# Kernel optimization log

Hardware: AMD Instinct MI355X
Metric: run time of the kernel (lower is better)

## Reference

```python
import jax, jax.numpy as jnp
import numpy as np

DIM = 128
NH = 4
K = 7
PAD = K // 2  # dilation = 1
MLP_HID = 4 * DIM
EPS = 1e-5


def _layernorm(x, w, b):
    m = jnp.mean(x, axis=-1, keepdims=True)
    v = jnp.mean((x - m) ** 2, axis=-1, keepdims=True)
    return (x - m) / jnp.sqrt(v + EPS) * w + b


def _windows(xp, H, W):
    # xp: [B, nh, Hp, Wp, hd] zero-padded; returns [B, nh, H, W, hd, K*K]
    return jnp.stack(
        [xp[:, :, i:i + H, j:j + W, :] for i in range(K) for j in range(K)],
        axis=-1,
    )


def setup_inputs() -> dict:
    key = jax.random.key(0)
    ks = jax.random.split(key, 10)
    s = 0.02
    inp = {
        "x": jax.random.normal(ks[0], (4, 56, 56, DIM), dtype=jnp.float32),
        "ln1_w": jnp.ones((DIM,), jnp.float32),
        "ln1_b": jnp.zeros((DIM,), jnp.float32),
        "w_qkv": jax.random.normal(ks[1], (DIM, 3 * DIM), jnp.float32) * s,
        "b_qkv": jnp.zeros((3 * DIM,), jnp.float32),
        "rpb": jax.random.normal(ks[2], (NH, K * K), jnp.float32) * s,
        "w_proj": jax.random.normal(ks[3], (DIM, DIM), jnp.float32) * s,
        "b_proj": jnp.zeros((DIM,), jnp.float32),
        "ln2_w": jnp.ones((DIM,), jnp.float32),
        "ln2_b": jnp.zeros((DIM,), jnp.float32),
        "w_fc1": jax.random.normal(ks[4], (DIM, MLP_HID), jnp.float32) * s,
        "b_fc1": jnp.zeros((MLP_HID,), jnp.float32),
        "w_fc2": jax.random.normal(ks[5], (MLP_HID, DIM), jnp.float32) * s,
        "b_fc2": jnp.zeros((DIM,), jnp.float32),
    }
    return inp


def _nat_block(x, ln1_w, ln1_b, w_qkv, b_qkv, rpb, w_proj, b_proj,
               ln2_w, ln2_b, w_fc1, b_fc1, w_fc2, b_fc2):
    B, H, W, C = x.shape
    hd = C // NH
    scale = hd ** -0.5

    # --- neighborhood attention ---
    xn = _layernorm(x, ln1_w, ln1_b)
    qkv = xn @ w_qkv + b_qkv                       # [B,H,W,3C]
    qkv = qkv.reshape(B, H, W, 3, NH, hd)
    qkv = jnp.transpose(qkv, (3, 0, 4, 1, 2, 5))   # [3,B,nh,H,W,hd]
    q, k, v = qkv[0] * scale, qkv[1], qkv[2]
    # zero-pad spatial dims (matches F.pad with constant 0 in original)
    pad = ((0, 0), (0, 0), (PAD, PAD), (PAD, PAD), (0, 0))
    kp = jnp.pad(k, pad)
    vp = jnp.pad(v, pad)
    kw = _windows(kp, H, W)                        # [B,nh,H,W,hd,49]
    vw = _windows(vp, H, W)
    attn = jnp.einsum('bnhwd,bnhwdk->bnhwk', q, kw)
    attn = attn + rpb[None, :, None, None, :]
    attn = jax.nn.softmax(attn, axis=-1)
    out = jnp.einsum('bnhwk,bnhwdk->bnhwd', attn, vw)  # [B,nh,H,W,hd]
    out = jnp.transpose(out, (0, 2, 3, 1, 4)).reshape(B, H, W, C)
    x = x + (out @ w_proj + b_proj)

    # --- MLP ---
    xn2 = _layernorm(x, ln2_w, ln2_b)
    h = jax.nn.gelu(xn2 @ w_fc1 + b_fc1, approximate=False)
    x = x + (h @ w_fc2 + b_fc2)
    return x


def reference(x, ln1_w, ln1_b, w_qkv, b_qkv, rpb, w_proj, b_proj,
              ln2_w, ln2_b, w_fc1, b_fc1, w_fc2, b_fc2):
    return _nat_block(x, ln1_w, ln1_b, w_qkv, b_qkv, rpb, w_proj, b_proj,
                      ln2_w, ln2_b, w_fc1, b_fc1, w_fc2, b_fc2)
```

## Files before the change

kernel.cpp:

```cpp
#include <hip/hip_runtime.h>

using bf16x8 = __attribute__((ext_vector_type(8))) short;
using f32x4  = __attribute__((ext_vector_type(4))) float;
typedef unsigned short u16;
typedef __attribute__((ext_vector_type(8))) unsigned short u16x8;

__device__ __forceinline__ u16 f2b(float f){
  unsigned int i=__float_as_uint(f);
  return (u16)((i + 0x7FFFu + ((i>>16)&1u))>>16);
}
__device__ __forceinline__ float b2f(u16 u){
  union{unsigned int i; float f;}v; v.i=((unsigned int)u)<<16; return v.f;
}
__device__ __forceinline__ void async16(const void* g, void* l){
  __builtin_amdgcn_global_load_lds((__attribute__((address_space(1))) void*)(g),
                                   (__attribute__((address_space(3))) void*)(l), 16, 0, 0);
}
__device__ __forceinline__ float gelu_tanh(float v){
  float u = v*(0.7978845608f + 0.0356774081f*v*v);
  float e = __expf(-2.0f*fabsf(u));
  float th = (1.0f-e)/(1.0f+e);
  th = (u<0.f)? -th : th;
  return 0.5f*v*(1.0f+th);
}

__global__ void prep_kernel(const float* __restrict__ wqkv, const float* __restrict__ wproj,
                            const float* __restrict__ wfc1, const float* __restrict__ wfc2,
                            u16* __restrict__ tqkv, u16* __restrict__ tproj,
                            u16* __restrict__ tfc1, u16* __restrict__ tfc2)
{
  int idx = blockIdx.x*256 + threadIdx.x;
  if (idx < 49152){ int n=idx>>7, k=idx&127; tqkv[idx]=f2b(wqkv[k*384+n]); }
  else if (idx < 65536){ int t=idx-49152; int n=t>>7, k=t&127; tproj[t]=f2b(wproj[k*128+n]); }
  else if (idx < 131072){ int t=idx-65536; int n=t>>7, k=t&127; tfc1[t]=f2b(wfc1[k*512+n]); }
  else if (idx < 196608){ int t=idx-131072; int n=t>>9, k=t&511; tfc2[t]=f2b(wfc2[k*128+n]); }
}

__global__ __launch_bounds__(256)
void qkv_ln_kernel(const float* __restrict__ x,
                   const float* __restrict__ ln1w, const float* __restrict__ ln1b,
                   const u16* __restrict__ tqkv, const float* __restrict__ bqkv,
                   u16* __restrict__ qb, u16* __restrict__ kb, u16* __restrict__ vb)
{
  __shared__ __align__(16) char smem[49152];
  char* lA = smem;
  char* lB = smem + 16384;

  const int tid = threadIdx.x;
  const int lane = tid&63, wid = tid>>6;
  const int quad = lane>>4, lrow = lane&15;
  const int m0 = blockIdx.x*64;
  const int wm = (wid&1)*32, wn = (wid>>1)*64;

  {
    const int row = tid>>2, q = tid&3;
    float xv[32];
    const float4* xr = (const float4*)(x + (size_t)(m0+row)*128 + q*32);
    float s=0.f, sq=0.f;
    #pragma unroll
    for (int c4=0;c4<8;c4++){
      float4 t = xr[c4];
      xv[c4*4]=t.x; xv[c4*4+1]=t.y; xv[c4*4+2]=t.z; xv[c4*4+3]=t.w;
      s += t.x+t.y+t.z+t.w;
      sq += t.x*t.x+t.y*t.y+t.z*t.z+t.w*t.w;
    }
    s  += __shfl_xor(s,1);  s  += __shfl_xor(s,2);
    sq += __shfl_xor(sq,1); sq += __shfl_xor(sq,2);
    float mean = s*0.0078125f;
    float rstd = rsqrtf(sq*0.0078125f - mean*mean + 1e-5f);
    const float4* wr = (const float4*)(ln1w + q*32);
    const float4* br = (const float4*)(ln1b + q*32);
    u16 nv[32];
    #pragma unroll
    for (int c4=0;c4<8;c4++){
      float4 w4 = wr[c4], b4 = br[c4];
      nv[c4*4]   = f2b((xv[c4*4]  -mean)*rstd*w4.x + b4.x);
      nv[c4*4+1] = f2b((xv[c4*4+1]-mean)*rstd*w4.y + b4.y);
      nv[c4*4+2] = f2b((xv[c4*4+2]-mean)*rstd*w4.z + b4.z);
      nv[c4*4+3] = f2b((xv[c4*4+3]-mean)*rstd*w4.w + b4.w);
    }
    #pragma unroll
    for (int cc=0;cc<4;cc++){
      u16x8 pk;
      #pragma unroll
      for (int e=0;e<8;e++) pk[e] = nv[cc*8+e];
      *(u16x8*)(lA + (((q*4+cc)*64 + row)<<4)) = pk;
    }
  }

  for (int nc=0; nc<3; nc++){
    __syncthreads();
    #pragma unroll
    for (int kk=0;kk<8;kk++){
      int i = tid + kk*256;
      int n = i&127, c = i>>7;
      async16(tqkv + (size_t)(nc*128+n)*128 + c*8, lB + i*16);
    }
    __syncthreads();

    f32x4 acc[2][4] = {};
    #pragma unroll
    for (int ks=0;ks<4;ks++){
      bf16x8 af[2], bfr[4];
      #pragma unroll
      for (int i=0;i<2;i++) af[i]  = ((const bf16x8*)lA)[(ks*4+quad)*64  + wm + i*16 + lrow];
      #pragma unroll
      for (int j=0;j<4;j++) bfr[j] = ((const bf16x8*)lB)[(ks*4+quad)*128 + wn + j*16 + lrow];
      #pragma unroll
      for (int i=0;i<2;i++)
        #pragma unroll
        for (int j=0;j<4;j++)
          acc[i][j] = __builtin_amdgcn_mfma_f32_16x16x32_bf16(af[i], bfr[j], acc[i][j], 0,0,0);
    }

    const float scale = 0.17677669529663687f;
    u16* dst = (nc==0)? qb : ((nc==1)? kb : vb);
    #pragma unroll
    for (int j=0;j<4;j++){
      int col = wn + j*16 + lrow;
      float bia = bqkv[nc*128 + col];
      #pragma unroll
      for (int i=0;i<2;i++){
        #pragma unroll
        for (int r=0;r<4;r++){
          int row = m0 + wm + i*16 + quad*4 + r;
          float val = acc[i][j][r] + bia;
          if (nc==0) val *= scale;
          dst[(size_t)row*128 + col] = f2b(val);
        }
      }
    }
  }
}

__global__ __launch_bounds__(256)
void attn_kernel(const u16* __restrict__ qb, const u16* __restrict__ kb,
                 const u16* __restrict__ vb, const float* __restrict__ rpb,
                 u16* __restrict__ aout)
{
  __shared__ __align__(16) u16 kt[196*32];
  __shared__ __align__(16) u16 vt[196*32];

  const int tid = threadIdx.x;
  const int tile = blockIdx.x;
  const int bh = blockIdx.y;
  const int b = bh>>2, h = bh&3;
  const int ty = (tile/7)*8, tx = (tile%7)*8;

  #pragma unroll
  for (int k=0;k<4;k++){
    int i = tid + k*256;
    if (i < 784){
      int pos = i>>2, c = i&3;
      int ly = pos/14, lx = pos-ly*14;
      int gy = ty + ly - 3, gx = tx + lx - 3;
      float4 kv = {0,0,0,0}, vv = {0,0,0,0};
      if (gy>=0 && gy<56 && gx>=0 && gx<56){
        size_t base = ((size_t)(b*3136 + gy*56 + gx)*128 + h*32 + c*8);
        kv = *(const float4*)(kb + base);
        vv = *(const float4*)(vb + base);
      }
      ((float4*)kt)[i] = kv;
      ((float4*)vt)[i] = vv;
    }
  }
  __syncthreads();

  const int px = tid>>2, q = tid&3;
  const int ly = px>>3, lx = px&7;
  const int tok = b*3136 + (ty+ly)*56 + (tx+lx);
  const int nbase = (ly*14 + lx)*32 + q*8;

  float qv[8];
  { u16x8 qq = *(const u16x8*)(qb + (size_t)tok*128 + h*32 + q*8);
    #pragma unroll
    for (int i=0;i<8;i++) qv[i]=b2f(qq[i]); }

  float sc[49];
  #pragma unroll
  for (int ky=0;ky<7;ky++){
    #pragma unroll
    for (int kx=0;kx<7;kx++){
      int n = ky*7+kx;
      u16x8 kk = *(const u16x8*)(kt + nbase + (ky*14+kx)*32);
      float s = 0.f;
      #pragma unroll
      for (int i=0;i<8;i++) s += qv[i]*b2f(kk[i]);
      s += __shfl_xor(s,1); s += __shfl_xor(s,2);
      sc[n] = s + rpb[h*49+n];
    }
  }
  float m=-1e30f;
  #pragma unroll
  for (int n=0;n<49;n++) m = fmaxf(m, sc[n]);
  float l=0.f;
  #pragma unroll
  for (int n=0;n<49;n++){ sc[n]=__expf(sc[n]-m); l+=sc[n]; }
  float inv = 1.f/l;

  float o[8]={};
  #pragma unroll
  for (int ky=0;ky<7;ky++){
    #pragma unroll
    for (int kx=0;kx<7;kx++){
      int n = ky*7+kx;
      u16x8 vv = *(const u16x8*)(vt + nbase + (ky*14+kx)*32);
      float p = sc[n];
      #pragma unroll
      for (int i=0;i<8;i++) o[i] += p*b2f(vv[i]);
    }
  }
  u16x8 ov;
  #pragma unroll
  for (int i=0;i<8;i++) ov[i] = f2b(o[i]*inv);
  *(u16x8*)(aout + (size_t)tok*128 + h*32 + q*8) = ov;
}

__global__ __launch_bounds__(256)
void mega_mlp_kernel(const u16* __restrict__ aout, const float* __restrict__ x,
                     const u16* __restrict__ tproj, const float* __restrict__ bproj,
                     const float* __restrict__ ln2w, const float* __restrict__ ln2b,
                     const u16* __restrict__ tfc1, const float* __restrict__ bfc1,
                     const u16* __restrict__ tfc2, const float* __restrict__ bfc2,
                     float* __restrict__ out)
{
  __shared__ __align__(16) char smem[65536];
  char* lA  = smem;
  char* lB  = smem + 16384;
  char* xn2 = smem + 49152;

  const int tid = threadIdx.x;
  const int lane = tid&63, wid = tid>>6;
  const int quad = lane>>4, lrow = lane&15;
  const int m0 = blockIdx.x*64;
  const int wm = (wid&1)*32, wn = (wid>>1)*64;
  const int half = wid>>1;

  #pragma unroll
  for (int kk=0;kk<4;kk++){
    int i = tid + kk*256;
    int row = i&63, c = i>>6;
    async16(aout + (size_t)(m0+row)*128 + c*8, lA + i*16);
  }
  #pragma unroll
  for (int kk=0;kk<8;kk++){
    int i = tid + kk*256;
    int n = i&127, c = i>>7;
    async16(tproj + (size_t)n*128 + c*8, lB + i*16);
  }
  __syncthreads();

  f32x4 acc[2][4] = {};
  #pragma unroll
  for (int ks=0;ks<4;ks++){
    bf16x8 af[2], bfr[4];
    #pragma unroll
    for (int i=0;i<2;i++) af[i]  = ((const bf16x8*)lA)[(ks*4+quad)*64  + wm + i*16 + lrow];
    #pragma unroll
    for (int j=0;j<4;j++) bfr[j] = ((const bf16x8*)lB)[(ks*4+quad)*128 + wn + j*16 + lrow];
    #pragma unroll
    for (int i=0;i<2;i++)
      #pragma unroll
      for (int j=0;j<4;j++)
        acc[i][j] = __builtin_amdgcn_mfma_f32_16x16x32_bf16(af[i], bfr[j], acc[i][j], 0,0,0);
  }
  __syncthreads();

  float x1v[2][4][4];
  float ps[2][4] = {}, pq[2][4] = {};
  #pragma unroll
  for (int j=0;j<4;j++){
    int col = wn + j*16 + lrow;
    float bia = bproj[col];
    #pragma unroll
    for (int i=0;i<2;i++){
      #pragma unroll
      for (int r=0;r<4;r++){
        int row = m0 + wm + i*16 + quad*4 + r;
        float val = acc[i][j][r] + bia + x[(size_t)row*128 + col];
        x1v[i][j][r] = val;
        ps[i][r] += val; pq[i][r] += val*val;
      }
    }
  }
  #pragma unroll
  for (int i=0;i<2;i++)
    #pragma unroll
    for (int r=0;r<4;r++){
      #pragma unroll
      for (int off=1; off<16; off<<=1){
        ps[i][r] += __shfl_xor(ps[i][r], off);
        pq[i][r] += __shfl_xor(pq[i][r], off);
      }
    }
  float* redS = (float*)lA;
  float* redQ = redS + 128;
  if (lrow==0){
    #pragma unroll
    for (int i=0;i<2;i++)
      #pragma unroll
      for (int r=0;r<4;r++){
        int row = wm + i*16 + quad*4 + r;
        redS[half*64 + row] = ps[i][r];
        redQ[half*64 + row] = pq[i][r];
      }
  }
  __syncthreads();

  {
    float w2[4], b2[4];
    #pragma unroll
    for (int j=0;j<4;j++){ int col = wn+j*16+lrow; w2[j]=ln2w[col]; b2[j]=ln2b[col]; }
    #pragma unroll
    for (int i=0;i<2;i++){
      #pragma unroll
      for (int r=0;r<4;r++){
        int row = wm + i*16 + quad*4 + r;
        float mean = (redS[row] + redS[64+row])*0.0078125f;
        float var  = (redQ[row] + redQ[64+row])*0.0078125f - mean*mean;
        float rstd = rsqrtf(var + 1e-5f);
        #pragma unroll
        for (int j=0;j<4;j++){
          int col = wn + j*16 + lrow;
          u16 hv = f2b((x1v[i][j][r]-mean)*rstd*w2[j] + b2[j]);
          ((u16*)xn2)[((col>>3)*64 + row)*8 + (col&7)] = hv;
        }
      }
    }
  }
  __syncthreads();

  f32x4 acc3[2][4] = {};
  for (int nc=0; nc<4; nc++){
    if (nc>0) __syncthreads();
    #pragma unroll
    for (int kk=0;kk<8;kk++){
      int i = tid + kk*256;
      int n = i&127, c = i>>7;
      async16(tfc1 + (size_t)(nc*128+n)*128 + c*8, lB + i*16);
    }
    __syncthreads();

    f32x4 acc2[2][4] = {};
    #pragma unroll
    for (int ks=0;ks<4;ks++){
      bf16x8 af[2], bfr[4];
      #pragma unroll
      for (int i=0;i<2;i++) af[i]  = ((const bf16x8*)xn2)[(ks*4+quad)*64  + wm + i*16 + lrow];
      #pragma unroll
      for (int j=0;j<4;j++) bfr[j] = ((const bf16x8*)lB)[(ks*4+quad)*128 + wn + j*16 + lrow];
      #pragma unroll
      for (int i=0;i<2;i++)
        #pragma unroll
        for (int j=0;j<4;j++)
          acc2[i][j] = __builtin_amdgcn_mfma_f32_16x16x32_bf16(af[i], bfr[j], acc2[i][j], 0,0,0);
    }
    #pragma unroll
    for (int j=0;j<4;j++){
      int col = wn + j*16 + lrow;
      float bia = bfc1[nc*128 + col];
      #pragma unroll
      for (int i=0;i<2;i++){
        #pragma unroll
        for (int r=0;r<4;r++){
          int row = wm + i*16 + quad*4 + r;
          float g = gelu_tanh(acc2[i][j][r] + bia);
          ((u16*)lA)[((col>>3)*64 + row)*8 + (col&7)] = f2b(g);
        }
      }
    }
    __syncthreads();
    #pragma unroll
    for (int kk=0;kk<8;kk++){
      int i = tid + kk*256;
      int n = i&127, c = i>>7;
      async16(tfc2 + (size_t)n*512 + nc*128 + c*8, lB + i*16);
    }
    __syncthreads();

    #pragma unroll
    for (int ks=0;ks<4;ks++){
      bf16x8 af[2], bfr[4];
      #pragma unroll
      for (int i=0;i<2;i++) af[i]  = ((const bf16x8*)lA)[(ks*4+quad)*64  + wm + i*16 + lrow];
      #pragma unroll
      for (int j=0;j<4;j++) bfr[j] = ((const bf16x8*)lB)[(ks*4+quad)*128 + wn + j*16 + lrow];
      #pragma unroll
      for (int i=0;i<2;i++)
        #pragma unroll
        for (int j=0;j<4;j++)
          acc3[i][j] = __builtin_amdgcn_mfma_f32_16x16x32_bf16(af[i], bfr[j], acc3[i][j], 0,0,0);
    }
  }

  #pragma unroll
  for (int j=0;j<4;j++){
    int col = wn + j*16 + lrow;
    float bia = bfc2[col];
    #pragma unroll
    for (int i=0;i<2;i++){
      #pragma unroll
      for (int r=0;r<4;r++){
        int row = m0 + wm + i*16 + quad*4 + r;
        out[(size_t)row*128 + col] = acc3[i][j][r] + bia + x1v[i][j][r];
      }
    }
  }
}

extern "C" void kernel_launch(void* const* d_in, const int* in_sizes, int n_in,
                              void* d_out, int out_size, void* d_ws, size_t ws_size,
                              hipStream_t stream)
{
  const float* x     =(const float*)d_in[0];
  const float* ln1w  =(const float*)d_in[1];
  const float* ln1b  =(const float*)d_in[2];
  const float* wqkv  =(const float*)d_in[3];
  const float* bqkv  =(const float*)d_in[4];
  const float* rpb   =(const float*)d_in[5];
  const float* wproj =(const float*)d_in[6];
  const float* bproj =(const float*)d_in[7];
  const float* ln2w  =(const float*)d_in[8];
  const float* ln2b  =(const float*)d_in[9];
  const float* wfc1  =(const float*)d_in[10];
  const float* bfc1  =(const float*)d_in[11];
  const float* wfc2  =(const float*)d_in[12];
  const float* bfc2  =(const float*)d_in[13];

  char* ws=(char*)d_ws;
  size_t o=0;
  u16* tqkv =(u16*)(ws+o); o+=98304;
  u16* tproj=(u16*)(ws+o); o+=32768;
  u16* tfc1 =(u16*)(ws+o); o+=131072;
  u16* tfc2 =(u16*)(ws+o); o+=131072;
  u16* aout =(u16*)(ws+o); o+=3211264;
  u16* qb   =(u16*)(ws+o); o+=3211264;
  u16* kb   =(u16*)(ws+o); o+=3211264;
  u16* vb   =(u16*)(ws+o); o+=3211264;

  prep_kernel<<<768,256,0,stream>>>(wqkv,wproj,wfc1,wfc2,tqkv,tproj,tfc1,tfc2);
  qkv_ln_kernel<<<196,256,0,stream>>>(x,ln1w,ln1b,tqkv,bqkv,qb,kb,vb);
  attn_kernel<<<dim3(49,16),256,0,stream>>>(qb,kb,vb,rpb,aout);
  mega_mlp_kernel<<<196,256,0,stream>>>(aout,x,tproj,bproj,ln2w,ln2b,
                                        tfc1,bfc1,tfc2,bfc2,(float*)d_out);
}
```

Measured before the change: 158.0 us.

## Compute neighborhood attention with MFMA over a banded 2-row halo window

Rewrites the neighborhood attention kernel so each wavefront handles 16 query pixels (two tile rows) and computes QK^T and PV with bf16 MFMA against the 112 halo positions those rows can reach. Out-of-window positions are masked to -inf before softmax, and probabilities are staged in LDS as bf16. V is stored transposed with padded strides so it can feed the MFMA B operand. This replaces scalar FMA dot products and shuffle reductions with matrix instructions. In exchange it does redundant masked work, about 112 candidate positions per query instead of 49, and adds the cost of LDS transposes and rounding P to bf16.

Measured after the change: 142.3 us. 1.11x faster.

```diff
diff --git a/kernel.cpp b/kernel.cpp
--- a/kernel.cpp
+++ b/kernel.cpp
@@ -4,6 +4,7 @@
 using f32x4  = __attribute__((ext_vector_type(4))) float;
 typedef unsigned short u16;
 typedef __attribute__((ext_vector_type(8))) unsigned short u16x8;
+typedef __attribute__((ext_vector_type(4))) unsigned short u16x4;
 
 __device__ __forceinline__ u16 f2b(float f){
   unsigned int i=__float_as_uint(f);
@@ -133,87 +134,137 @@
   }
 }
 
+#define KT_S 40
+#define VT_S 232
+#define P_S  152
 __global__ __launch_bounds__(256)
 void attn_kernel(const u16* __restrict__ qb, const u16* __restrict__ kb,
                  const u16* __restrict__ vb, const float* __restrict__ rpb,
                  u16* __restrict__ aout)
 {
-  __shared__ __align__(16) u16 kt[196*32];
-  __shared__ __align__(16) u16 vt[196*32];
+  __shared__ __align__(16) char smem[50192];
+  u16*  kt   = (u16*)smem;
+  u16*  vt   = (u16*)(smem + 15680);
+  u16*  Pm   = (u16*)(smem + 30528);
+  float* srpb= (float*)(smem + 49984);
 
   const int tid = threadIdx.x;
-  const int tile = blockIdx.x;
-  const int bh = blockIdx.y;
+  const int tile = blockIdx.x, bh = blockIdx.y;
   const int b = bh>>2, h = bh&3;
   const int ty = (tile/7)*8, tx = (tile%7)*8;
-
-  #pragma unroll
-  for (int k=0;k<4;k++){
-    int i = tid + k*256;
+  const int lane = tid&63, wid = tid>>6;
+  const int quad = lane>>4, lrow = lane&15;
+
+  #pragma unroll
+  for (int kk=0;kk<4;kk++){
+    int i = tid + kk*256;
     if (i < 784){
-      int pos = i>>2, c = i&3;
-      int ly = pos/14, lx = pos-ly*14;
-      int gy = ty + ly - 3, gx = tx + lx - 3;
-      float4 kv = {0,0,0,0}, vv = {0,0,0,0};
-      if (gy>=0 && gy<56 && gx>=0 && gx<56){
-        size_t base = ((size_t)(b*3136 + gy*56 + gx)*128 + h*32 + c*8);
-        kv = *(const float4*)(kb + base);
-        vv = *(const float4*)(vb + base);
-      }
-      ((float4*)kt)[i] = kv;
-      ((float4*)vt)[i] = vv;
-    }
-  }
-  __syncthreads();
-
-  const int px = tid>>2, q = tid&3;
-  const int ly = px>>3, lx = px&7;
-  const int tok = b*3136 + (ty+ly)*56 + (tx+lx);
-  const int nbase = (ly*14 + lx)*32 + q*8;
-
-  float qv[8];
-  { u16x8 qq = *(const u16x8*)(qb + (size_t)tok*128 + h*32 + q*8);
-    #pragma unroll
-    for (int i=0;i<8;i++) qv[i]=b2f(qq[i]); }
-
-  float sc[49];
-  #pragma unroll
-  for (int ky=0;ky<7;ky++){
-    #pragma unroll
-    for (int kx=0;kx<7;kx++){
-      int n = ky*7+kx;
-      u16x8 kk = *(const u16x8*)(kt + nbase + (ky*14+kx)*32);
-      float s = 0.f;
-      #pragma unroll
-      for (int i=0;i<8;i++) s += qv[i]*b2f(kk[i]);
-      s += __shfl_xor(s,1); s += __shfl_xor(s,2);
-      sc[n] = s + rpb[h*49+n];
-    }
-  }
-  float m=-1e30f;
-  #pragma unroll
-  for (int n=0;n<49;n++) m = fmaxf(m, sc[n]);
-  float l=0.f;
-  #pragma unroll
-  for (int n=0;n<49;n++){ sc[n]=__expf(sc[n]-m); l+=sc[n]; }
-  float inv = 1.f/l;
-
-  float o[8]={};
-  #pragma unroll
-  for (int ky=0;ky<7;ky++){
-    #pragma unroll
-    for (int kx=0;kx<7;kx++){
-      int n = ky*7+kx;
-      u16x8 vv = *(const u16x8*)(vt + nbase + (ky*14+kx)*32);
-      float p = sc[n];
-      #pragma unroll
-      for (int i=0;i<8;i++) o[i] += p*b2f(vv[i]);
-    }
-  }
-  u16x8 ov;
-  #pragma unroll
-  for (int i=0;i<8;i++) ov[i] = f2b(o[i]*inv);
-  *(u16x8*)(aout + (size_t)tok*128 + h*32 + q*8) = ov;
+      int pos = i>>2, oct = i&3;
+      int hy = pos/14, hx = pos - hy*14;
+      int gy = ty + hy - 3, gx = tx + hx - 3;
+      u16x8 kv = {0,0,0,0,0,0,0,0};
+      if (gy>=0 && gy<56 && gx>=0 && gx<56)
+        kv = *(const u16x8*)(kb + ((size_t)(b*3136 + gy*56 + gx)*128 + h*32 + oct*8));
+      *(u16x8*)(kt + pos*KT_S + oct*8) = kv;
+    }
+  }
+  #pragma unroll
+  for (int kk=0;kk<4;kk++){
+    int i = tid + kk*256;
+    if (i < 896){
+      int pos = i>>2, oct = i&3;
+      u16x8 vv = {0,0,0,0,0,0,0,0};
+      if (pos < 196){
+        int hy = pos/14, hx = pos - hy*14;
+        int gy = ty + hy - 3, gx = tx + hx - 3;
+        if (gy>=0 && gy<56 && gx>=0 && gx<56)
+          vv = *(const u16x8*)(vb + ((size_t)(b*3136 + gy*56 + gx)*128 + h*32 + oct*8));
+      }
+      #pragma unroll
+      for (int j=0;j<8;j++) vt[(oct*8+j)*VT_S + pos] = vv[j];
+    }
+  }
+  if (tid < 49) srpb[tid] = rpb[h*49 + tid];
+  __syncthreads();
+
+  const int pxq = wid*16 + lrow;
+  const int tokq = b*3136 + (ty + (pxq>>3))*56 + tx + (pxq&7);
+  bf16x8 qf = *(const bf16x8*)(qb + (size_t)tokq*128 + h*32 + quad*8);
+
+  f32x4 sc[7];
+  const f32x4 zf = {0.f,0.f,0.f,0.f};
+  #pragma unroll
+  for (int cg=0;cg<7;cg++){
+    int pos = wid*28 + cg*16 + lrow;
+    bf16x8 kf = *(const bf16x8*)(kt + pos*KT_S + quad*8);
+    sc[cg] = __builtin_amdgcn_mfma_f32_16x16x32_bf16(qf, kf, zf, 0,0,0);
+  }
+
+  const int lyq = quad>>1;
+  #pragma unroll
+  for (int cg=0;cg<7;cg++){
+    int np = cg*16 + lrow;
+    int nh = np/14, hx = np - nh*14;
+    int dy = nh - lyq;
+    #pragma unroll
+    for (int r=0;r<4;r++){
+      int lx = (quad*4+r)&7;
+      int dx = hx - lx;
+      bool in = ((unsigned)dy<7u) && ((unsigned)dx<7u);
+      float bias = srpb[in ? (dy*7+dx) : 0];
+      sc[cg][r] = in ? (sc[cg][r] + bias) : -1e30f;
+    }
+  }
+  float rmax[4], lsum[4], inv[4];
+  #pragma unroll
+  for (int r=0;r<4;r++){
+    float m = sc[0][r];
+    #pragma unroll
+    for (int cg=1;cg<7;cg++) m = fmaxf(m, sc[cg][r]);
+    m = fmaxf(m, __shfl_xor(m,1)); m = fmaxf(m, __shfl_xor(m,2));
+    m = fmaxf(m, __shfl_xor(m,4)); m = fmaxf(m, __shfl_xor(m,8));
+    rmax[r] = m;
+    float l = 0.f;
+    #pragma unroll
+    for (int cg=0;cg<7;cg++){ float p = __expf(sc[cg][r]-m); sc[cg][r]=p; l+=p; }
+    l += __shfl_xor(l,1); l += __shfl_xor(l,2);
+    l += __shfl_xor(l,4); l += __shfl_xor(l,8);
+    lsum[r]=l; inv[r]=1.f/l;
+  }
+
+  u16* Pw = Pm + wid*16*P_S;
+  #pragma unroll
+  for (int cg=0;cg<7;cg++){
+    int np = cg*16 + lrow;
+    #pragma unroll
+    for (int r=0;r<4;r++)
+      Pw[(quad*4+r)*P_S + np] = f2b(sc[cg][r]);
+  }
+  { int zr = lane>>2, seg = lane&3;
+    u16x4 z4 = {0,0,0,0};
+    *(u16x4*)(Pw + zr*P_S + 112 + seg*4) = z4; }
+  __syncthreads();
+
+  f32x4 oacc[2] = {zf, zf};
+  #pragma unroll
+  for (int ks=0;ks<4;ks++){
+    bf16x8 pf = *(const bf16x8*)(Pw + lrow*P_S + ks*32 + quad*8);
+    #pragma unroll
+    for (int cg2=0;cg2<2;cg2++){
+      bf16x8 vf = *(const bf16x8*)(vt + (cg2*16+lrow)*VT_S + wid*28 + ks*32 + quad*8);
+      oacc[cg2] = __builtin_amdgcn_mfma_f32_16x16x32_bf16(pf, vf, oacc[cg2], 0,0,0);
+    }
+  }
+  #pragma unroll
+  for (int r=0;r<4;r++){
+    int px = wid*16 + quad*4 + r;
+    int tok = b*3136 + (ty + (px>>3))*56 + tx + (px&7);
+    #pragma unroll
+    for (int cg2=0;cg2<2;cg2++){
+      int ch = cg2*16 + lrow;
+      aout[(size_t)tok*128 + h*32 + ch] = f2b(oacc[cg2][r]*inv[r]);
+    }
+  }
 }
 
 __global__ __launch_bounds__(256)
```
